# Kernel tuning notes

Hardware: AMD Instinct MI355X
Metric: run time of the kernel (lower is better)

The kernel has to match this reference:

```python
import jax, jax.numpy as jnp
import numpy as np

N, D, H = 2048, 1024, 16
HD = D // H  # 64
SCALE = float(np.sqrt(HD))  # sqrt(features // heads) = 8.0


def setup_inputs() -> dict:
    key = jax.random.key(0)
    ks = jax.random.split(key, 9)
    s = 0.02
    return {
        "x": jax.random.normal(ks[0], (N, D), dtype=jnp.float32),
        "Wq": jax.random.normal(ks[1], (D, D), dtype=jnp.float32) * s,
        "bq": jnp.zeros((D,), dtype=jnp.float32),
        "Wk": jax.random.normal(ks[2], (D, D), dtype=jnp.float32) * s,
        "bk": jnp.zeros((D,), dtype=jnp.float32),
        "Wv": jax.random.normal(ks[3], (D, D), dtype=jnp.float32) * s,
        "bv": jnp.zeros((D,), dtype=jnp.float32),
        "Wo": jax.random.normal(ks[4], (D, D), dtype=jnp.float32) * s,
        "bo": jnpp if False else jnp.zeros((D,), dtype=jnp.float32),
    }


def reference(x, Wq, bq, Wk, bk, Wv, bv, Wo, bo):
    # projections: [n, d]
    q = x @ Wq + bq
    k = x @ Wk + bk
    v = x @ Wv + bv
    # split heads: n (h d) -> h n d
    def split(t):
        return t.reshape(N, H, HD).transpose(1, 0, 2)
    q, k, v = split(q), split(k), split(v)
    # attention scores [h, n, n]
    scores = jnp.einsum('hnd,hmd->hnm', q, k) / SCALE
    # causal mask (tril), fill with dtype min as in original
    dmin = jnp.finfo(scores.dtype).min
    mask = jnp.tril(jnp.ones((N, N), dtype=bool))
    scores = jnp.where(mask, scores, dmin)
    attn = jax.nn.softmax(scores, axis=-1)
    # weighted sum, merge heads: h n d -> n (h d)
    out = jnp.einsum('hnm,hmd->hnd', attn, v)
    out = out.transpose(1, 0, 2).reshape(N, D)
    return out @ Wo + bo
```

## Files before the change

kernel.cpp:

```cpp
#include <hip/hip_runtime.h>
#include <hip/hip_bf16.h>
#include <math.h>

#define SA_N 2048
#define SA_D 1024
#define SA_H 16
#define SA_HD 64

typedef __attribute__((ext_vector_type(8))) short bf16x8;
typedef __attribute__((ext_vector_type(4))) float f32x4;
typedef __attribute__((address_space(3))) void lds_t;
typedef __attribute__((address_space(1))) void gmem_t;

__global__ __launch_bounds__(256) void cvt_bf16_kernel(
    const float* __restrict__ in, __hip_bfloat16* __restrict__ out, int n4)
{
    int i = blockIdx.x * 256 + threadIdx.x;
    if (i < n4) {
        float4 v = reinterpret_cast<const float4*>(in)[i];
        union { __hip_bfloat16 hh[4]; short4 s4; } u;
        u.hh[0] = __float2bfloat16(v.x);
        u.hh[1] = __float2bfloat16(v.y);
        u.hh[2] = __float2bfloat16(v.z);
        u.hh[3] = __float2bfloat16(v.w);
        reinterpret_cast<short4*>(out)[i] = u.s4;
    }
}

__global__ __launch_bounds__(256) void cvtT4_kernel(
    const float* __restrict__ W0, const float* __restrict__ W1,
    const float* __restrict__ W2, const float* __restrict__ W3,
    __hip_bfloat16* __restrict__ WtAll)
{
    const int z = blockIdx.z;
    const float* W = (z == 0) ? W0 : (z == 1) ? W1 : (z == 2) ? W2 : W3;
    __hip_bfloat16* Wt = WtAll + (size_t)z * SA_D * SA_D;
    __shared__ float t[32][33];
    const int c0 = blockIdx.x * 32, r0 = blockIdx.y * 32;
    const int tx = threadIdx.x & 31, ty = threadIdx.x >> 5;
#pragma unroll
    for (int p = 0; p < 4; ++p)
        t[ty + p * 8][tx] = W[(size_t)(r0 + ty + p * 8) * SA_D + c0 + tx];
    __syncthreads();
#pragma unroll
    for (int p = 0; p < 4; ++p)
        Wt[(size_t)(c0 + ty + p * 8) * SA_D + r0 + tx] = __float2bfloat16(t[tx][ty + p * 8]);
}

__device__ __forceinline__ void gemm_body_128x64(
    const __hip_bfloat16* __restrict__ A,
    const __hip_bfloat16* __restrict__ Bt,
    const float* __restrict__ bias,
    void* __restrict__ Cout, int mode, int M, int Kdim, int Nout,
    char* As, char* Bs)
{
    const int tid = threadIdx.x;
    const int wave = tid >> 6, lane = tid & 63;
    const int m = lane & 15, quad = lane >> 4;
    const int wm = wave >> 1, wn = wave & 1;
    const int row0 = blockIdx.y * 128, col0 = blockIdx.x * 64;

    f32x4 acc[4][2];
#pragma unroll
    for (int i = 0; i < 4; ++i)
#pragma unroll
        for (int j = 0; j < 2; ++j) acc[i][j] = (f32x4){0.f, 0.f, 0.f, 0.f};

    const int sr = tid >> 3;
    const int sc = tid & 7;

    for (int k0 = 0; k0 < Kdim; k0 += 64) {
#pragma unroll
        for (int p = 0; p < 4; ++p) {
            const int r = p * 32 + sr;
            const int pc = (sc ^ (r & 7)) * 16;
            const char* ga = (const char*)(A + (size_t)(row0 + r) * Kdim + k0) + pc;
            __builtin_amdgcn_global_load_lds((gmem_t*)ga,
                (lds_t*)(As + p * 4096 + wave * 1024), 16, 0, 0);
        }
#pragma unroll
        for (int p = 0; p < 2; ++p) {
            const int r = p * 32 + sr;
            const int pc = (sc ^ (r & 7)) * 16;
            const char* gb = (const char*)(Bt + (size_t)(col0 + r) * Kdim + k0) + pc;
            __builtin_amdgcn_global_load_lds((gmem_t*)gb,
                (lds_t*)(Bs + p * 4096 + wave * 1024), 16, 0, 0);
        }
        __syncthreads();

#pragma unroll
        for (int s = 0; s < 2; ++s) {
            bf16x8 af[4], bfr[2];
#pragma unroll
            for (int mi = 0; mi < 4; ++mi) {
                const int row = wm * 64 + mi * 16 + m;
                const int pc = (s * 4 + quad) ^ (row & 7);
                af[mi] = *reinterpret_cast<const bf16x8*>(As + row * 128 + pc * 16);
            }
#pragma unroll
            for (int ni = 0; ni < 2; ++ni) {
                const int col = wn * 32 + ni * 16 + m;
                const int pc = (s * 4 + quad) ^ (col & 7);
                bfr[ni] = *reinterpret_cast<const bf16x8*>(Bs + col * 128 + pc * 16);
            }
#pragma unroll
            for (int mi = 0; mi < 4; ++mi)
#pragma unroll
                for (int ni = 0; ni < 2; ++ni)
                    acc[mi][ni] = __builtin_amdgcn_mfma_f32_16x16x32_bf16(
                        af[mi], bfr[ni], acc[mi][ni], 0, 0, 0);
        }
        __syncthreads();
    }

#pragma unroll
    for (int ni = 0; ni < 2; ++ni) {
        const int col = col0 + wn * 32 + ni * 16 + m;
        const float bv = bias[col];
#pragma unroll
        for (int mi = 0; mi < 4; ++mi) {
            const int rbase = row0 + wm * 64 + mi * 16 + quad * 4;
            if (mode == 0) {
#pragma unroll
                for (int reg = 0; reg < 4; ++reg)
                    ((float*)Cout)[(size_t)(rbase + reg) * Nout + col] =
                        acc[mi][ni][reg] + bv;
            } else if (mode == 1) {
#pragma unroll
                for (int reg = 0; reg < 4; ++reg)
                    ((__hip_bfloat16*)Cout)[(size_t)(rbase + reg) * Nout + col] =
                        __float2bfloat16(acc[mi][ni][reg] + bv);
            } else {
                union { __hip_bfloat16 hh[4]; short4 s4; } u;
#pragma unroll
                for (int reg = 0; reg < 4; ++reg)
                    u.hh[reg] = __float2bfloat16(acc[mi][ni][reg] + bv);
                *reinterpret_cast<short4*>(
                    &((__hip_bfloat16*)Cout)[(size_t)col * M + rbase]) = u.s4;
            }
        }
    }
}

__global__ __launch_bounds__(256) void gemm_qkv_kernel(
    const __hip_bfloat16* __restrict__ xbf, const __hip_bfloat16* __restrict__ WtAll,
    const float* __restrict__ bq, const float* __restrict__ bk, const float* __restrict__ bv,
    __hip_bfloat16* __restrict__ Qb, __hip_bfloat16* __restrict__ Kb,
    __hip_bfloat16* __restrict__ VtT)
{
    __shared__ __align__(16) char As[128 * 128];
    __shared__ __align__(16) char Bs[64 * 128];
    const int z = blockIdx.z;
    const __hip_bfloat16* Bt = WtAll + (size_t)z * SA_D * SA_D;
    const float* bias = (z == 0) ? bq : (z == 1) ? bk : bv;
    void* out = (z == 0) ? (void*)Qb : (z == 1) ? (void*)Kb : (void*)VtT;
    gemm_body_128x64(xbf, Bt, bias, out, (z == 2) ? 2 : 1, SA_N, SA_D, SA_D, As, Bs);
}

__global__ __launch_bounds__(256) void gemm_out_kernel(
    const __hip_bfloat16* __restrict__ Abf, const __hip_bfloat16* __restrict__ Wt,
    const float* __restrict__ bo, float* __restrict__ out)
{
    __shared__ __align__(16) char As[128 * 128];
    __shared__ __align__(16) char Bs[64 * 128];
    gemm_body_128x64(Abf, Wt, bo, out, 0, SA_N, SA_D, SA_D, As, Bs);
}

__global__ __launch_bounds__(256) void flash_mfma_kernel(
    const __hip_bfloat16* __restrict__ Qb,
    const __hip_bfloat16* __restrict__ Kb,
    const __hip_bfloat16* __restrict__ Vt,
    __hip_bfloat16* __restrict__ O)
{
    const int b = blockIdx.x;
    const int h = b & 15;
    const int qraw = b >> 4;
    const int qt = (qraw < 16) ? qraw : 47 - qraw;
    const int row0 = qt * 64;

    const int tid = threadIdx.x;
    const int wave = tid >> 6, lane = tid & 63;
    const int ln = lane & 15, quad = lane >> 4;

    __shared__ __align__(16) char Qs[64 * 128];
    __shared__ __align__(16) char Ks[2][64 * 128];
    __shared__ __align__(16) char Vs[2][64 * 128];
    __shared__ __align__(16) char Ps[64 * 144];

    const int sr = tid >> 3;
    const int sc = tid & 7;

#pragma unroll
    for (int p = 0; p < 2; ++p) {
        const int r = p * 32 + sr;
        const int pc = (sc ^ (r & 7)) * 16;
        const char* gq = (const char*)(Qb + (size_t)(row0 + r) * SA_D + h * SA_HD) + pc;
        __builtin_amdgcn_global_load_lds((gmem_t*)gq,
            (lds_t*)(Qs + p * 4096 + wave * 1024), 16, 0, 0);
    }

    auto stage = [&](int kt, int bb) {
#pragma unroll
        for (int p = 0; p < 2; ++p) {
            const int r = p * 32 + sr;
            const int pc = (sc ^ (r & 7)) * 16;
            const char* gk = (const char*)(Kb + (size_t)(kt * 64 + r) * SA_D + h * SA_HD) + pc;
            __builtin_amdgcn_global_load_lds((gmem_t*)gk,
                (lds_t*)(Ks[bb] + p * 4096 + wave * 1024), 16, 0, 0);
            const char* gv = (const char*)(Vt + (size_t)(h * SA_HD + r) * SA_N + kt * 64) + pc;
            __builtin_amdgcn_global_load_lds((gmem_t*)gv,
                (lds_t*)(Vs[bb] + p * 4096 + wave * 1024), 16, 0, 0);
        }
    };
    stage(0, 0);

    f32x4 oacc[4], lacc;
#pragma unroll
    for (int g = 0; g < 4; ++g) oacc[g] = (f32x4){0.f, 0.f, 0.f, 0.f};
    lacc = (f32x4){0.f, 0.f, 0.f, 0.f};

    const float sc2 = 0.18033688011112042f;
    const short one_bf = (short)0x3F80;
    const bf16x8 ones = {one_bf, one_bf, one_bf, one_bf, one_bf, one_bf, one_bf, one_bf};

    for (int kt = 0; kt <= qt; ++kt) {
        __syncthreads();
        if (kt < qt) stage(kt + 1, (kt + 1) & 1);
        const char* K_ = Ks[kt & 1];
        const char* V_ = Vs[kt & 1];

        f32x4 sacc[4];
#pragma unroll
        for (int g = 0; g < 4; ++g) sacc[g] = (f32x4){0.f, 0.f, 0.f, 0.f};
        const int mrow = wave * 16 + ln;
#pragma unroll
        for (int s = 0; s < 2; ++s) {
            const int pca = (s * 4 + quad) ^ (mrow & 7);
            bf16x8 af = *reinterpret_cast<const bf16x8*>(Qs + mrow * 128 + pca * 16);
#pragma unroll
            for (int g = 0; g < 4; ++g) {
                const int krow = g * 16 + ln;
                const int pcb = (s * 4 + quad) ^ (krow & 7);
                bf16x8 bf = *reinterpret_cast<const bf16x8*>(K_ + krow * 128 + pcb * 16);
                sacc[g] = __builtin_amdgcn_mfma_f32_16x16x32_bf16(af, bf, sacc[g], 0, 0, 0);
            }
        }

        const bool last = (kt == qt);
        const int prow_b = wave * 16 + quad * 4;
        const int qrow_b = row0 + prow_b;
#pragma unroll
        for (int g = 0; g < 4; ++g) {
            const int key = kt * 64 + g * 16 + ln;
#pragma unroll
            for (int reg = 0; reg < 4; ++reg) {
                float p = exp2f(sacc[g][reg] * sc2);
                if (last && key > (qrow_b + reg)) p = 0.f;
                *reinterpret_cast<__hip_bfloat16*>(
                    Ps + (prow_b + reg) * 144 + (g * 16 + ln) * 2) = __float2bfloat16(p);
            }
        }

#pragma unroll
        for (int s2 = 0; s2 < 2; ++s2) {
            bf16x8 pf = *reinterpret_cast<const bf16x8*>(
                Ps + (wave * 16 + ln) * 144 + s2 * 64 + quad * 16);
            lacc = __builtin_amdgcn_mfma_f32_16x16x32_bf16(pf, ones, lacc, 0, 0, 0);
#pragma unroll
            for (int dg = 0; dg < 4; ++dg) {
                const int vrow = dg * 16 + ln;
                const int pcb = ((s2 * 4 + quad) ^ (vrow & 7)) * 16;
                bf16x8 vf = *reinterpret_cast<const bf16x8*>(V_ + vrow * 128 + pcb);
                oacc[dg] = __builtin_amdgcn_mfma_f32_16x16x32_bf16(pf, vf, oacc[dg], 0, 0, 0);
            }
        }
    }

#pragma unroll
    for (int reg = 0; reg < 4; ++reg) {
        const int qrow = row0 + wave * 16 + quad * 4 + reg;
        const float inv = 1.0f / lacc[reg];
#pragma unroll
        for (int dg = 0; dg < 4; ++dg)
            O[(size_t)qrow * SA_D + h * SA_HD + dg * 16 + ln] =
                __float2bfloat16(oacc[dg][reg] * inv);
    }
}

extern "C" void kernel_launch(void* const* d_in, const int* in_sizes, int n_in,
                              void* d_out, int out_size, void* d_ws, size_t ws_size,
                              hipStream_t stream) {
    const float* x  = (const float*)d_in[0];
    const float* Wq = (const float*)d_in[1];
    const float* bq = (const float*)d_in[2];
    const float* Wk = (const float*)d_in[3];
    const float* bk = (const float*)d_in[4];
    const float* Wv = (const float*)d_in[5];
    const float* bv = (const float*)d_in[6];
    const float* Wo = (const float*)d_in[7];
    const float* bo = (const float*)d_in[8];
    float* out = (float*)d_out;

    const size_t ND = (size_t)SA_N * SA_D;
    const size_t DD = (size_t)SA_D * SA_D;
    __hip_bfloat16* xbf   = (__hip_bfloat16*)d_ws;
    __hip_bfloat16* WtAll = xbf + ND;
    __hip_bfloat16* Qb    = WtAll + 4 * DD;
    __hip_bfloat16* Kb    = Qb + ND;
    __hip_bfloat16* VtT   = Kb + ND;
    __hip_bfloat16* Abf   = VtT + ND;

    cvt_bf16_kernel<<<dim3((unsigned)(ND / 4 / 256)), 256, 0, stream>>>(x, xbf, (int)(ND / 4));
    cvtT4_kernel<<<dim3(SA_D / 32, SA_D / 32, 4), 256, 0, stream>>>(Wq, Wk, Wv, Wo, WtAll);
    gemm_qkv_kernel<<<dim3(SA_D / 64, SA_N / 128, 3), 256, 0, stream>>>(
        xbf, WtAll, bq, bk, bv, Qb, Kb, VtT);
    flash_mfma_kernel<<<dim3(512), 256, 0, stream>>>(Qb, Kb, VtT, Abf);
    gemm_out_kernel<<<dim3(SA_D / 64, SA_N / 128), 256, 0, stream>>>(
        Abf, WtAll + 3 * DD, bo, out);
}
```

Measured before the change: 163.1 us.

## Fuse prep kernels, fold softmax scale into Wq, shrink GEMM tiles to 64x64

Merges the x conversion and weight transpose into one prep kernel, saving a launch. Pre-multiplies Wq and bq by the exp2 softmax scale, which removes a multiply per score in the flash kernel. Shrinks the GEMM tiles from 128x64 to 64x64, doubling the block count for better CU occupancy on a 256-CU part. The cost is less operand reuse per block and a small bf16 rounding change from scaling before conversion.

After: 154.5 us. -5.3%, faster.

```diff
diff --git a/kernel.cpp b/kernel.cpp
--- a/kernel.cpp
+++ b/kernel.cpp
@@ -12,45 +12,50 @@
 typedef __attribute__((address_space(3))) void lds_t;
 typedef __attribute__((address_space(1))) void gmem_t;
 
-__global__ __launch_bounds__(256) void cvt_bf16_kernel(
-    const float* __restrict__ in, __hip_bfloat16* __restrict__ out, int n4)
-{
-    int i = blockIdx.x * 256 + threadIdx.x;
-    if (i < n4) {
-        float4 v = reinterpret_cast<const float4*>(in)[i];
+#define SC2 0.18033688011112042f
+
+__global__ __launch_bounds__(256) void prep_kernel(
+    const float* __restrict__ x,
+    const float* __restrict__ Wq, const float* __restrict__ Wk,
+    const float* __restrict__ Wv, const float* __restrict__ Wo,
+    __hip_bfloat16* __restrict__ xbf, __hip_bfloat16* __restrict__ WtAll)
+{
+    const int tid = threadIdx.x;
+    const int z = blockIdx.z;
+    if (z < 2) {
+        const int r = z * 1024 + blockIdx.y * 32 + (tid >> 3);
+        const int c = blockIdx.x * 32 + (tid & 7) * 4;
+        const size_t idx = (size_t)r * SA_D + c;
+        float4 v = *reinterpret_cast<const float4*>(&x[idx]);
         union { __hip_bfloat16 hh[4]; short4 s4; } u;
         u.hh[0] = __float2bfloat16(v.x);
         u.hh[1] = __float2bfloat16(v.y);
         u.hh[2] = __float2bfloat16(v.z);
         u.hh[3] = __float2bfloat16(v.w);
-        reinterpret_cast<short4*>(out)[i] = u.s4;
-    }
-}
-
-__global__ __launch_bounds__(256) void cvtT4_kernel(
-    const float* __restrict__ W0, const float* __restrict__ W1,
-    const float* __restrict__ W2, const float* __restrict__ W3,
-    __hip_bfloat16* __restrict__ WtAll)
-{
-    const int z = blockIdx.z;
-    const float* W = (z == 0) ? W0 : (z == 1) ? W1 : (z == 2) ? W2 : W3;
-    __hip_bfloat16* Wt = WtAll + (size_t)z * SA_D * SA_D;
-    __shared__ float t[32][33];
-    const int c0 = blockIdx.x * 32, r0 = blockIdx.y * 32;
-    const int tx = threadIdx.x & 31, ty = threadIdx.x >> 5;
-#pragma unroll
-    for (int p = 0; p < 4; ++p)
-        t[ty + p * 8][tx] = W[(size_t)(r0 + ty + p * 8) * SA_D + c0 + tx];
-    __syncthreads();
-#pragma unroll
-    for (int p = 0; p < 4; ++p)
-        Wt[(size_t)(c0 + ty + p * 8) * SA_D + r0 + tx] = __float2bfloat16(t[tx][ty + p * 8]);
-}
-
-__device__ __forceinline__ void gemm_body_128x64(
+        *reinterpret_cast<short4*>(&xbf[idx]) = u.s4;
+    } else {
+        const int w = z - 2;
+        const float* W = (w == 0) ? Wq : (w == 1) ? Wk : (w == 2) ? Wv : Wo;
+        const float scale = (w == 0) ? SC2 : 1.0f;
+        __hip_bfloat16* Wt = WtAll + (size_t)w * SA_D * SA_D;
+        __shared__ float t[32][33];
+        const int c0 = blockIdx.x * 32, r0 = blockIdx.y * 32;
+        const int tx = tid & 31, ty = tid >> 5;
+#pragma unroll
+        for (int p = 0; p < 4; ++p)
+            t[ty + p * 8][tx] = W[(size_t)(r0 + ty + p * 8) * SA_D + c0 + tx] * scale;
+        __syncthreads();
+#pragma unroll
+        for (int p = 0; p < 4; ++p)
+            Wt[(size_t)(c0 + ty + p * 8) * SA_D + r0 + tx] =
+                __float2bfloat16(t[tx][ty + p * 8]);
+    }
+}
+
+__device__ __forceinline__ void gemm_tile_body(
     const __hip_bfloat16* __restrict__ A,
     const __hip_bfloat16* __restrict__ Bt,
-    const float* __restrict__ bias,
+    const float* __restrict__ bias, float bias_scale,
     void* __restrict__ Cout, int mode, int M, int Kdim, int Nout,
     char* As, char* Bs)
 {
@@ -58,11 +63,11 @@
     const int wave = tid >> 6, lane = tid & 63;
     const int m = lane & 15, quad = lane >> 4;
     const int wm = wave >> 1, wn = wave & 1;
-    const int row0 = blockIdx.y * 128, col0 = blockIdx.x * 64;
-
-    f32x4 acc[4][2];
-#pragma unroll
-    for (int i = 0; i < 4; ++i)
+    const int row0 = blockIdx.y * 64, col0 = blockIdx.x * 64;
+
+    f32x4 acc[2][2];
+#pragma unroll
+    for (int i = 0; i < 2; ++i)
 #pragma unroll
         for (int j = 0; j < 2; ++j) acc[i][j] = (f32x4){0.f, 0.f, 0.f, 0.f};
 
@@ -71,17 +76,12 @@
 
     for (int k0 = 0; k0 < Kdim; k0 += 64) {
 #pragma unroll
-        for (int p = 0; p < 4; ++p) {
+        for (int p = 0; p < 2; ++p) {
             const int r = p * 32 + sr;
             const int pc = (sc ^ (r & 7)) * 16;
             const char* ga = (const char*)(A + (size_t)(row0 + r) * Kdim + k0) + pc;
             __builtin_amdgcn_global_load_lds((gmem_t*)ga,
                 (lds_t*)(As + p * 4096 + wave * 1024), 16, 0, 0);
-        }
-#pragma unroll
-        for (int p = 0; p < 2; ++p) {
-            const int r = p * 32 + sr;
-            const int pc = (sc ^ (r & 7)) * 16;
             const char* gb = (const char*)(Bt + (size_t)(col0 + r) * Kdim + k0) + pc;
             __builtin_amdgcn_global_load_lds((gmem_t*)gb,
                 (lds_t*)(Bs + p * 4096 + wave * 1024), 16, 0, 0);
@@ -90,10 +90,10 @@
 
 #pragma unroll
         for (int s = 0; s < 2; ++s) {
-            bf16x8 af[4], bfr[2];
-#pragma unroll
-            for (int mi = 0; mi < 4; ++mi) {
-                const int row = wm * 64 + mi * 16 + m;
+            bf16x8 af[2], bfr[2];
+#pragma unroll
+            for (int mi = 0; mi < 2; ++mi) {
+                const int row = wm * 32 + mi * 16 + m;
                 const int pc = (s * 4 + quad) ^ (row & 7);
                 af[mi] = *reinterpret_cast<const bf16x8*>(As + row * 128 + pc * 16);
             }
@@ -104,7 +104,7 @@
                 bfr[ni] = *reinterpret_cast<const bf16x8*>(Bs + col * 128 + pc * 16);
             }
 #pragma unroll
-            for (int mi = 0; mi < 4; ++mi)
+            for (int mi = 0; mi < 2; ++mi)
 #pragma unroll
                 for (int ni = 0; ni < 2; ++ni)
                     acc[mi][ni] = __builtin_amdgcn_mfma_f32_16x16x32_bf16(
@@ -116,10 +116,10 @@
 #pragma unroll
     for (int ni = 0; ni < 2; ++ni) {
         const int col = col0 + wn * 32 + ni * 16 + m;
-        const float bv = bias[col];
-#pragma unroll
-        for (int mi = 0; mi < 4; ++mi) {
-            const int rbase = row0 + wm * 64 + mi * 16 + quad * 4;
+        const float bv = bias[col] * bias_scale;
+#pragma unroll
+        for (int mi = 0; mi < 2; ++mi) {
+            const int rbase = row0 + wm * 32 + mi * 16 + quad * 4;
             if (mode == 0) {
 #pragma unroll
                 for (int reg = 0; reg < 4; ++reg)
@@ -148,22 +148,23 @@
     __hip_bfloat16* __restrict__ Qb, __hip_bfloat16* __restrict__ Kb,
     __hip_bfloat16* __restrict__ VtT)
 {
-    __shared__ __align__(16) char As[128 * 128];
+    __shared__ __align__(16) char As[64 * 128];
     __shared__ __align__(16) char Bs[64 * 128];
     const int z = blockIdx.z;
     const __hip_bfloat16* Bt = WtAll + (size_t)z * SA_D * SA_D;
     const float* bias = (z == 0) ? bq : (z == 1) ? bk : bv;
     void* out = (z == 0) ? (void*)Qb : (z == 1) ? (void*)Kb : (void*)VtT;
-    gemm_body_128x64(xbf, Bt, bias, out, (z == 2) ? 2 : 1, SA_N, SA_D, SA_D, As, Bs);
+    gemm_tile_body(xbf, Bt, bias, (z == 0) ? SC2 : 1.0f, out,
+                   (z == 2) ? 2 : 1, SA_N, SA_D, SA_D, As, Bs);
 }
 
 __global__ __launch_bounds__(256) void gemm_out_kernel(
     const __hip_bfloat16* __restrict__ Abf, const __hip_bfloat16* __restrict__ Wt,
     const float* __restrict__ bo, float* __restrict__ out)
 {
-    __shared__ __align__(16) char As[128 * 128];
+    __shared__ __align__(16) char As[64 * 128];
     __shared__ __align__(16) char Bs[64 * 128];
-    gemm_body_128x64(Abf, Wt, bo, out, 0, SA_N, SA_D, SA_D, As, Bs);
+    gemm_tile_body(Abf, Wt, bo, 1.0f, out, 0, SA_N, SA_D, SA_D, As, Bs);
 }
 
 __global__ __launch_bounds__(256) void flash_mfma_kernel(
@@ -219,7 +220,6 @@
     for (int g = 0; g < 4; ++g) oacc[g] = (f32x4){0.f, 0.f, 0.f, 0.f};
     lacc = (f32x4){0.f, 0.f, 0.f, 0.f};
 
-    const float sc2 = 0.18033688011112042f;
     const short one_bf = (short)0x3F80;
     const bf16x8 ones = {one_bf, one_bf, one_bf, one_bf, one_bf, one_bf, one_bf, one_bf};
 
@@ -254,7 +254,7 @@
             const int key = kt * 64 + g * 16 + ln;
 #pragma unroll
             for (int reg = 0; reg < 4; ++reg) {
-                float p = exp2f(sacc[g][reg] * sc2);
+                float p = exp2f(sacc[g][reg]);
                 if (last && key > (qrow_b + reg)) p = 0.f;
                 *reinterpret_cast<__hip_bfloat16*>(
                     Ps + (prow_b + reg) * 144 + (g * 16 + ln) * 2) = __float2bfloat16(p);
@@ -310,11 +310,10 @@
     __hip_bfloat16* VtT   = Kb + ND;
     __hip_bfloat16* Abf   = VtT + ND;
 
-    cvt_bf16_kernel<<<dim3((unsigned)(ND / 4 / 256)), 256, 0, stream>>>(x, xbf, (int)(ND / 4));
-    cvtT4_kernel<<<dim3(SA_D / 32, SA_D / 32, 4), 256, 0, stream>>>(Wq, Wk, Wv, Wo, WtAll);
-    gemm_qkv_kernel<<<dim3(SA_D / 64, SA_N / 128, 3), 256, 0, stream>>>(
+    prep_kernel<<<dim3(32, 32, 6), 256, 0, stream>>>(x, Wq, Wk, Wv, Wo, xbf, WtAll);
+    gemm_qkv_kernel<<<dim3(SA_D / 64, SA_N / 64, 3), 256, 0, stream>>>(
         xbf, WtAll, bq, bk, bv, Qb, Kb, VtT);
     flash_mfma_kernel<<<dim3(512), 256, 0, stream>>>(Qb, Kb, VtT, Abf);
-    gemm_out_kernel<<<dim3(SA_D / 64, SA_N / 128), 256, 0, stream>>>(
+    gemm_out_kernel<<<dim3(SA_D / 64, SA_N / 64), 256, 0, stream>>>(
         Abf, WtAll + 3 * DD, bo, out);
 }
```
